# Kernel optimization log

Measured on AMD Instinct MI355X. Metric: run time of the kernel, lower is better.

## Reference

```python
import jax, jax.numpy as jnp
import numpy as np

EMB_DIM, TREE_DIM, OUT_DIM, VOCAB = 256, 256, 3, 10000
T, B, LEVELS = 255, 128, 8  # complete binary tree of depth 8, 128 trees per input


def _build_forest():
    # node j = T-1-heap(j): root (heap 0) is the LAST node so stack_last_h picks the root.
    heap = np.arange(T)
    depth = np.floor(np.log2(heap + 1)).astype(np.int64)  # 0..7
    node_order = np.empty(T, dtype=np.int64)
    node_order[T - 1 - heap] = (LEVELS - 1) - depth       # leaves=0, root=7
    internal = np.arange((T - 1) // 2)                     # heaps with two children
    parent = np.repeat(T - 1 - internal, 2)
    child = np.stack([T - 1 - (2 * internal + 1), T - 1 - (2 * internal + 2)], 1).reshape(-1)
    edges = np.stack([parent, child], axis=1)              # (254, 2)
    edge_order = node_order[parent]
    offs = (np.arange(B) * T)[:, None, None]
    adj = (edges[None] + offs).reshape(-1, 2)              # (B*254, 2)
    return np.tile(node_order, B), adj, np.tile(edge_order, B)


def setup_inputs() -> dict:
    key = jax.random.key(0)
    ks = jax.random.split(key, 16)
    no, adj, eo = _build_forest()
    D = TREE_DIM
    s_e = 1.0 / np.sqrt(EMB_DIM)
    s_t = 1.0 / np.sqrt(D)
    return {
        'feat_cube': jax.random.randint(ks[0], (B * T,), 0, VOCAB),
        'feat_a': jax.random.randint(ks[1], (B * T,), 0, VOCAB),
        'feat_b': jax.random.randint(ks[2], (B * T,), 0, VOCAB),
        'node_order': jnp.asarray(no),
        'adjacency_list': jnp.asarray(adj),
        'edge_order': jnp.asarray(eo),
        'num_levels': LEVELS,
        'num_trees': B,
        'emb': jax.random.normal(ks[3], (VOCAB, EMB_DIM), jnp.float32),
        'W_iou': jax.random.normal(ks[4], (3 * D, EMB_DIM), jnp.float32) * s_e,
        'b_iou': jnp.zeros((3 * D,), jnp.float32),
        'U_iou': jax.random.normal(ks[5], (3 * D, D), jnp.float32) * s_t,
        'W_f': jax.random.normal(ks[6], (D, EMB_DIM), jnp.float32) * s_e,
        'b_f': jnp.zeros((D,), jnp.float32),
        'U_f': jax.random.normal(ks[7], (D, D), jnp.float32) * s_t,
        'fc1_w': jax.random.normal(ks[8], (D // 2, D), jnp.float32) * s_t,
        'fc1_b': jnp.zeros((D // 2,), jnp.float32),
        'fc2_w': jax.random.normal(ks[9], (OUT_DIM, D // 2), jnp.float32) * (1.0 / np.sqrt(D // 2)),
        'fc2_b': jnp.zeros((OUT_DIM,), jnp.float32),
    }


def _tree_lstm(x, node_order, parents, children, edge_order, W_iou, b_iou, U_iou, W_f, b_f, U_f, num_levels):
    # Child-sum TreeLSTM, evaluated level by level (leaves first). Dense masked
    # formulation: per level we update only nodes with node_order==lvl; edge
    # contributions are masked before segment_sum (same math as the torch loop).
    N = x.shape[0]
    D = U_f.shape[0]
    x_iou = x @ W_iou.T + b_iou            # (N, 3D), precomputed once
    x_f = x @ W_f.T + b_f                  # (N, D)
    h = jnp.zeros((N, D), x.dtype)
    c = jnp.zeros((N, D), x.dtype)
    for lvl in range(num_levels):
        emask = (edge_order == lvl)[:, None].astype(x.dtype)
        ch = h[children]                   # (E, D) gather of child hidden
        cc = c[children]
        f = jax.nn.sigmoid(x_f[parents] + ch @ U_f.T)
        h_sum = jax.ops.segment_sum(ch * emask, parents, num_segments=N)
        c_sum = jax.ops.segment_sum(f * cc * emask, parents, num_segments=N)
        i, o, u = jnp.split(x_iou + h_sum @ U_iou.T, 3, axis=1)
        c_new = jax.nn.sigmoid(i) * jnp.tanh(u) + c_sum
        h_new = jax.nn.sigmoid(o) * jnp.tanh(c_new)
        nmask = (node_order == lvl)[:, None]
        h = jnp.where(nmask, h_new, h)
        c = jnp.where(nmask, c_new, c)
    return h, c


def reference(feat_cube, feat_a, feat_b, node_order, adjacency_list, edge_order,
              num_levels, num_trees, emb, W_iou, b_iou, U_iou, W_f, b_f, U_f,
              fc1_w, fc1_b, fc2_w, fc2_b):
    parents = adjacency_list[:, 0]
    children = adjacency_list[:, 1]

    def run_tree(feat):
        h, _ = _tree_lstm(emb[feat], node_order, parents, children, edge_order,
                          W_iou, b_iou, U_iou, W_f, b_f, U_f, num_levels)
        # stack_last_h: last node of each tree (= root with our labeling)
        return h.reshape(num_trees, -1, h.shape[-1])[:, -1, :]

    h_c = run_tree(feat_cube)
    h_a = run_tree(feat_a)
    h_b = run_tree(feat_b)
    # h_c (1,D) @ (h_a (D,1) @ h_b (1,D)) == (h_c . h_a) * h_b, fused einsum
    h = jnp.einsum('bi,bi,bj->bj', h_c, h_a, h_b)
    hid = jax.nn.relu(h @ fc1_w.T + fc1_b)
    logits = jax.nn.relu(hid @ fc2_w.T + fc2_b)
    return logits  # (num_trees, out_dim)
```

## Files before the change

### kernel.cpp

```cpp
#include <hip/hip_runtime.h>
#include <hip/hip_bf16.h>

typedef __hip_bfloat16 bf16;
typedef unsigned short u16;
typedef __attribute__((ext_vector_type(8))) short s8;
typedef __attribute__((ext_vector_type(4))) float f4;

#define NRUNS 3
#define NTREE 128
#define TT    255
#define DD    256
#define VPAD  10016
#define PAD   258

__device__ __forceinline__ float bits2f(u16 b){ union{unsigned u; float f;} x; x.u = ((unsigned)b)<<16; return x.f; }
__device__ __forceinline__ u16   f2bits(float f){ bf16 h = __float2bfloat16(f); return *(u16*)&h; }
__device__ __forceinline__ float sigm(float x){ return 1.f/(1.f+__expf(-x)); }
__device__ __forceinline__ float tanh_(float x){ return 1.f - 2.f/(__expf(2.f*x)+1.f); }

__global__ void k_detect(const u16* __restrict__ raw, int* __restrict__ flag){
    int t = threadIdx.x;
    int hit = 0;
    if (t < 128){
        u16 w = raw[2*t];
        int e = (w >> 7) & 0xFF;
        hit = (e >= 100 && e <= 141) ? 1 : 0;
    }
    __shared__ int cnt;
    if (t == 0) cnt = 0;
    __syncthreads();
    atomicAdd(&cnt, hit);
    __syncthreads();
    if (t == 0) flag[0] = (cnt >= 64) ? 1 : 0;
}

__device__ __forceinline__ u16 cvt1b(const void* p, int i, int isb){
    return isb ? ((const u16*)p)[i] : f2bits(((const float*)p)[i]);
}
__device__ __forceinline__ float cvt1f(const void* p, int i, int isb){
    return isb ? bits2f(((const u16*)p)[i]) : ((const float*)p)[i];
}

#define L_EMB  (10000*256)
#define L_EMBP (VPAD*256)
#define L_WIOU (768*256)
#define L_UIOU (768*256)
#define L_WF   (256*256)
#define L_UF   (256*256)
#define L_ALL  (L_EMBP + L_WIOU + L_UIOU + L_WF + L_UF)
#define S_BIOU 768
#define S_BF   256
#define S_F1W  (128*256)
#define S_F1B  128
#define S_F2W  (3*128)
#define S_F2B  3
#define S_ALL  (S_BIOU+S_BF+S_F1W+S_F1B+S_F2W+S_F2B)
__global__ void k_cvtall(const void* __restrict__ s0, const void* __restrict__ s1,
                         const void* __restrict__ s2, const void* __restrict__ s3,
                         const void* __restrict__ s4,
                         const void* __restrict__ t0, const void* __restrict__ t1,
                         const void* __restrict__ t2, const void* __restrict__ t3,
                         const void* __restrict__ t4, const void* __restrict__ t5,
                         u16* __restrict__ d0, u16* __restrict__ d1, u16* __restrict__ d2,
                         u16* __restrict__ d3, u16* __restrict__ d4,
                         float* __restrict__ e0, float* __restrict__ e1, float* __restrict__ e2,
                         float* __restrict__ e3, float* __restrict__ e4, float* __restrict__ e5,
                         const int* __restrict__ flag){
    int isb = flag[0];
    for (int i = blockIdx.x*blockDim.x + threadIdx.x; i < L_ALL + S_ALL; i += gridDim.x*blockDim.x){
        int j = i;
        if (j < L_EMBP){ d0[j] = (j < L_EMB) ? cvt1b(s0, j, isb) : (u16)0; continue; } j -= L_EMBP;
        if (j < L_WIOU){ d1[j] = cvt1b(s1, j, isb); continue; } j -= L_WIOU;
        if (j < L_UIOU){ d2[j] = cvt1b(s2, j, isb); continue; } j -= L_UIOU;
        if (j < L_WF){ d3[j] = cvt1b(s3, j, isb); continue; } j -= L_WF;
        if (j < L_UF){ d4[j] = cvt1b(s4, j, isb); continue; } j -= L_UF;
        if (j < S_BIOU){ e0[j] = cvt1f(t0, j, isb); continue; } j -= S_BIOU;
        if (j < S_BF){ e1[j] = cvt1f(t1, j, isb); continue; } j -= S_BF;
        if (j < S_F1W){ e2[j] = cvt1f(t2, j, isb); continue; } j -= S_F1W;
        if (j < S_F1B){ e3[j] = cvt1f(t3, j, isb); continue; } j -= S_F1B;
        if (j < S_F2W){ e4[j] = cvt1f(t4, j, isb); continue; } j -= S_F2W;
        e5[j] = cvt1f(t5, j, isb);
    }
}

__device__ __forceinline__ s8 ldB16(const u16* p){
    union { uint4 q; s8 v; } u;
    u.q = *(const uint4*)p;
    return u.v;
}
__device__ __forceinline__ s8 ldsA(const u16* p){
    union { unsigned w[4]; s8 v; } u;
    u.w[0] = *(const unsigned*)(p);
    u.w[1] = *(const unsigned*)(p+2);
    u.w[2] = *(const unsigned*)(p+4);
    u.w[3] = *(const unsigned*)(p+6);
    return u.v;
}
#define MFMA(acc,a,b) acc = __builtin_amdgcn_mfma_f32_16x16x32_bf16(a, b, acc, 0, 0, 0)

__global__ __launch_bounds__(512, 4)
void k_vocab2(const u16* __restrict__ embb,
              const u16* __restrict__ Wiou, const u16* __restrict__ Wfm,
              const u16* __restrict__ Ufm,  const float* __restrict__ biou_f,
              u16* __restrict__ E_iou, u16* __restrict__ E_f,
              u16* __restrict__ H0, u16* __restrict__ C0, u16* __restrict__ HU0)
{
    __shared__ u16 hs[32*PAD];
    const int t = threadIdx.x, w = t>>6, lane = t&63, ln = lane&15, q = lane>>4;
    const int r0 = blockIdx.x*32, d0 = w*32;

    const u16* Bp[8];
    #pragma unroll
    for (int g = 0; g < 4; g++)
      #pragma unroll
      for (int nc = 0; nc < 2; nc++){
        int nn = d0 + nc*16 + ln;
        Bp[g*2+nc] = (g < 3) ? (Wiou + (size_t)(g*256+nn)*DD) : (Wfm + (size_t)nn*DD);
      }
    const u16* a0p = embb + (size_t)(r0+ln)*DD;
    const u16* a1p = embb + (size_t)(r0+16+ln)*DD;
    f4 acc[8][2];
    #pragma unroll
    for (int nt = 0; nt < 8; nt++){ acc[nt][0] = (f4){0,0,0,0}; acc[nt][1] = (f4){0,0,0,0}; }
    #pragma unroll 2
    for (int ks = 0; ks < 8; ks++){
        int ko = ks*32 + q*8;
        s8 a0 = ldB16(a0p + ko);
        s8 a1 = ldB16(a1p + ko);
        #pragma unroll
        for (int nt = 0; nt < 8; nt++){
            s8 bb = ldB16(Bp[nt] + ko);
            MFMA(acc[nt][0], a0, bb);
            MFMA(acc[nt][1], a1, bb);
        }
    }
    #pragma unroll
    for (int nc = 0; nc < 2; nc++){
        int d = d0 + nc*16 + ln;
        float bi = biou_f[d], bo = biou_f[256+d], bu = biou_f[512+d];
        #pragma unroll
        for (int ms = 0; ms < 2; ms++)
          #pragma unroll
          for (int r = 0; r < 4; r++){
            int vrow = r0 + ms*16 + q*4 + r;
            float ei = acc[0*2+nc][ms][r];
            float eo = acc[1*2+nc][ms][r];
            float eu = acc[2*2+nc][ms][r];
            float ef = acc[3*2+nc][ms][r];
            size_t eb = (size_t)vrow*768 + d;
            E_iou[eb]       = f2bits(ei);
            E_iou[eb + 256] = f2bits(eo);
            E_iou[eb + 512] = f2bits(eu);
            E_f[(size_t)vrow*DD + d] = f2bits(ef);
            float cc = sigm(ei + bi)*tanh_(eu + bu);
            float hh = sigm(eo + bo)*tanh_(cc);
            C0[(size_t)vrow*DD + d] = f2bits(cc);
            H0[(size_t)vrow*DD + d] = f2bits(hh);
            hs[(ms*16 + q*4 + r)*PAD + d] = f2bits(hh);
        }
    }
    __syncthreads();

    f4 hacc[2][2];
    #pragma unroll
    for (int nt = 0; nt < 2; nt++){ hacc[nt][0] = (f4){0,0,0,0}; hacc[nt][1] = (f4){0,0,0,0}; }
    const u16* Bf0 = Ufm + (size_t)(d0 + ln)*DD;
    const u16* Bf1 = Ufm + (size_t)(d0 + 16 + ln)*DD;
    #pragma unroll 2
    for (int ks = 0; ks < 8; ks++){
        int ko = ks*32 + q*8;
        s8 a0 = ldsA(&hs[ln*PAD + ko]);
        s8 a1 = ldsA(&hs[(16+ln)*PAD + ko]);
        s8 b0 = ldB16(Bf0 + ko);
        s8 b1 = ldB16(Bf1 + ko);
        MFMA(hacc[0][0], a0, b0); MFMA(hacc[0][1], a1, b0);
        MFMA(hacc[1][0], a0, b1); MFMA(hacc[1][1], a1, b1);
    }
    #pragma unroll
    for (int nc = 0; nc < 2; nc++){
        int d = d0 + nc*16 + ln;
        #pragma unroll
        for (int ms = 0; ms < 2; ms++)
          #pragma unroll
          for (int r = 0; r < 4; r++){
            int vrow = r0 + ms*16 + q*4 + r;
            HU0[(size_t)vrow*DD + d] = f2bits(hacc[nc][ms][r]);
        }
    }
}

__global__ __launch_bounds__(512, 4)
void k_lvl1(const int* __restrict__ f0, const int* __restrict__ f1, const int* __restrict__ f2,
            const u16* __restrict__ E_iou, const u16* __restrict__ E_f,
            const u16* __restrict__ H0, const u16* __restrict__ C0, const u16* __restrict__ HU0,
            const u16* __restrict__ Uiou, const u16* __restrict__ Ufm,
            const float* __restrict__ biou_f, const float* __restrict__ bf_f,
            u16* __restrict__ hsum_out, u16* __restrict__ fcsum_out)
{
    __shared__ u16 hs[32*PAD];
    const int t = threadIdx.x, w = t>>6, lane = t&63, ln = lane&15, q = lane>>4;
    const int r0 = blockIdx.x*32, d0 = w*32;

    const u16 *pa1[2], *pa2[2];
    #pragma unroll
    for (int ms = 0; ms < 2; ms++){
        int row = r0 + ms*16 + ln;
        int run = row >> 13, rem = row & 8191;
        int b = rem >> 6, jj = rem & 63;
        const int* fp = (run==0) ? f0 : ((run==1) ? f1 : f2);
        pa1[ms] = H0 + (size_t)fp[b*TT + 2*jj]*DD;
        pa2[ms] = H0 + (size_t)fp[b*TT + 2*jj + 1]*DD;
    }
    int fo[2][4], v1e[2][4], v2e[2][4], featp[2][2];
    #pragma unroll
    for (int ms = 0; ms < 2; ms++)
      #pragma unroll
      for (int r = 0; r < 4; r++){
        int rho = r0 + ms*16 + q*4 + r;
        int run = rho >> 13, rem = rho & 8191;
        int b = rem >> 6, jj = rem & 63;
        const int* fp = (run==0) ? f0 : ((run==1) ? f1 : f2);
        fo[ms][r]  = fp[b*TT + 128 + jj];
        v1e[ms][r] = fp[b*TT + 2*jj];
        v2e[ms][r] = fp[b*TT + 2*jj + 1];
        if ((r&1)==0) featp[ms][r>>1] = fp[b*TT + 192 + (jj>>1)];
      }

    f4 acc[6][2];
    #pragma unroll
    for (int nt = 0; nt < 6; nt++){ acc[nt][0] = (f4){0,0,0,0}; acc[nt][1] = (f4){0,0,0,0}; }
    {
        const u16* Bp[6];
        #pragma unroll
        for (int nt = 0; nt < 6; nt++){
            int n = (nt>>1)*256 + d0 + (nt&1)*16 + ln;
            Bp[nt] = Uiou + (size_t)n*DD;
        }
        #pragma unroll 2
        for (int ks = 0; ks < 8; ks++){
            int ko = ks*32 + q*8;
            s8 a10 = ldB16(pa1[0] + ko);
            s8 a11 = ldB16(pa1[1] + ko);
            s8 a20 = ldB16(pa2[0] + ko);
            s8 a21 = ldB16(pa2[1] + ko);
            #pragma unroll
            for (int nt = 0; nt < 6; nt++){
                s8 bb = ldB16(Bp[nt] + ko);
                MFMA(acc[nt][0], a10, bb);
                MFMA(acc[nt][0], a20, bb);
                MFMA(acc[nt][1], a11, bb);
                MFMA(acc[nt][1], a21, bb);
            }
        }
    }

    float cv[2][2][4];
    #pragma unroll
    for (int nc = 0; nc < 2; nc++){
        int d = d0 + nc*16 + ln;
        float bi = biou_f[d], bo = biou_f[256+d], bu = biou_f[512+d];
        float bfv = bf_f[d];
        #pragma unroll
        for (int ms = 0; ms < 2; ms++){
            float hv[4];
            #pragma unroll
            for (int r = 0; r < 4; r++){
                size_t eb = (size_t)fo[ms][r]*768 + d;
                float iv = acc[0+nc][ms][r] + bits2f(E_iou[eb])       + bi;
                float ov = acc[2+nc][ms][r] + bits2f(E_iou[eb + 256]) + bo;
                float uv = acc[4+nc][ms][r] + bits2f(E_iou[eb + 512]) + bu;
                float e  = bits2f(E_f[(size_t)fo[ms][r]*DD + d]) + bfv;
                size_t b1 = (size_t)v1e[ms][r]*DD + d;
                size_t b2 = (size_t)v2e[ms][r]*DD + d;
                float fa = sigm(e + bits2f(HU0[b1]));
                float fb = sigm(e + bits2f(HU0[b2]));
                float cs = fa*bits2f(C0[b1]) + fb*bits2f(C0[b2]);
                float c = sigm(iv)*tanh_(uv) + cs;
                float h = sigm(ov)*tanh_(c);
                cv[nc][ms][r] = c;
                hv[r] = h;
                hs[(ms*16 + q*4 + r)*PAD + d] = f2bits(h);
            }
            int prow = (r0>>1) + ms*8 + q*2;
            hsum_out[(size_t)prow*DD + d]     = f2bits(hv[0] + hv[1]);
            hsum_out[(size_t)(prow+1)*DD + d] = f2bits(hv[2] + hv[3]);
        }
    }

    __syncthreads();
    f4 hacc[2][2];
    #pragma unroll
    for (int nt = 0; nt < 2; nt++){ hacc[nt][0] = (f4){0,0,0,0}; hacc[nt][1] = (f4){0,0,0,0}; }
    const u16* Bf0 = Ufm + (size_t)(d0 + ln)*DD;
    const u16* Bf1 = Ufm + (size_t)(d0 + 16 + ln)*DD;
    #pragma unroll 2
    for (int ks = 0; ks < 8; ks++){
        int ko = ks*32 + q*8;
        s8 a0 = ldsA(&hs[ln*PAD + ko]);
        s8 a1 = ldsA(&hs[(16+ln)*PAD + ko]);
        s8 b0 = ldB16(Bf0 + ko);
        s8 b1 = ldB16(Bf1 + ko);
        MFMA(hacc[0][0], a0, b0); MFMA(hacc[0][1], a1, b0);
        MFMA(hacc[1][0], a0, b1); MFMA(hacc[1][1], a1, b1);
    }
    #pragma unroll
    for (int nc = 0; nc < 2; nc++){
        int d = d0 + nc*16 + ln;
        float bfv = bf_f[d];
        #pragma unroll
        for (int ms = 0; ms < 2; ms++){
            float fs0, fs1;
            #pragma unroll
            for (int r = 0; r < 4; r++){
                float ef = bits2f(E_f[(size_t)featp[ms][r>>1]*DD + d]);
                float fc = sigm(ef + bfv + hacc[nc][ms][r]) * cv[nc][ms][r];
                if (r == 0) fs0 = fc;
                else if (r == 1) fs0 += fc;
                else if (r == 2) fs1 = fc;
                else fs1 += fc;
            }
            int prow = (r0>>1) + ms*8 + q*2;
            fcsum_out[(size_t)prow*DD + d]     = f2bits(fs0);
            fcsum_out[(size_t)(prow+1)*DD + d] = f2bits(fs1);
        }
    }
}

__global__ __launch_bounds__(512, 4)
void k_lvl(int lvl, int cLog,
           const int* __restrict__ f0, const int* __restrict__ f1, const int* __restrict__ f2,
           const u16* __restrict__ E_iou, const u16* __restrict__ E_f,
           const u16* __restrict__ Uiou, const u16* __restrict__ Ufm,
           const float* __restrict__ biou_f, const float* __restrict__ bf_f,
           const u16* __restrict__ hsum_in, const u16* __restrict__ fcsum_in,
           u16* __restrict__ hsum_out, u16* __restrict__ fcsum_out,
           u16* __restrict__ hroot)
{
    __shared__ u16 hs[32*PAD];
    const int t = threadIdx.x, w = t>>6, lane = t&63, ln = lane&15, q = lane>>4;
    const int cnt = 1 << cLog, S = 256 - 2*cnt;
    const int r0 = blockIdx.x*32, d0 = w*32;
    const bool haveP = (lvl < 7);

    int feat[2][4], featp[2][2];
    #pragma unroll
    for (int ms = 0; ms < 2; ms++)
      #pragma unroll
      for (int r = 0; r < 4; r++){
        int rho = r0 + ms*16 + q*4 + r;
        int run = rho >> (7+cLog);
        int rem = rho & ((1<<(7+cLog)) - 1);
        int b = rem >> cLog, jj = rem & (cnt-1);
        const int* fp = (run==0) ? f0 : ((run==1) ? f1 : f2);
        feat[ms][r] = fp[b*TT + S + jj];
        if (haveP && (r&1)==0)
            featp[ms][r>>1] = fp[b*TT + (256-cnt) + (jj>>1)];
      }

    f4 acc[6][2];
    #pragma unroll
    for (int nt = 0; nt < 6; nt++){ acc[nt][0] = (f4){0,0,0,0}; acc[nt][1] = (f4){0,0,0,0}; }
    {
        const u16* a0p = hsum_in + (size_t)(r0+ln)*DD;
        const u16* a1p = hsum_in + (size_t)(r0+16+ln)*DD;
        const u16* Bp[6];
        #pragma unroll
        for (int nt = 0; nt < 6; nt++){
            int n = (nt>>1)*256 + d0 + (nt&1)*16 + ln;
            Bp[nt] = Uiou + (size_t)n*DD;
        }
        #pragma unroll 2
        for (int ks = 0; ks < 8; ks++){
            int ko = ks*32 + q*8;
            s8 a0 = ldB16(a0p + ko);
            s8 a1 = ldB16(a1p + ko);
            #pragma unroll
            for (int nt = 0; nt < 6; nt++){
                s8 bb = ldB16(Bp[nt] + ko);
                MFMA(acc[nt][0], a0, bb);
                MFMA(acc[nt][1], a1, bb);
            }
        }
    }

    float cv[2][2][4];
    #pragma unroll
    for (int nc = 0; nc < 2; nc++){
        int d = d0 + nc*16 + ln;
        float bi = biou_f[d], bo = biou_f[256+d], bu = biou_f[512+d];
        #pragma unroll
        for (int ms = 0; ms < 2; ms++){
            float hv[4];
            #pragma unroll
            for (int r = 0; r < 4; r++){
                int rho = r0 + ms*16 + q*4 + r;
                size_t eb = (size_t)feat[ms][r]*768 + d;
                float iv = acc[0+nc][ms][r] + bits2f(E_iou[eb])       + bi;
                float ov = acc[2+nc][ms][r] + bits2f(E_iou[eb + 256]) + bo;
                float uv = acc[4+nc][ms][r] + bits2f(E_iou[eb + 512]) + bu;
                float cs = bits2f(fcsum_in[(size_t)rho*DD + d]);
                float c = sigm(iv)*tanh_(uv) + cs;
                float h = sigm(ov)*tanh_(c);
                cv[nc][ms][r] = c;
                hv[r] = h;
                if (haveP) hs[(ms*16 + q*4 + r)*PAD + d] = f2bits(h);
                else       hroot[(size_t)rho*DD + d] = f2bits(h);
            }
            if (haveP){
                int prow = (r0>>1) + ms*8 + q*2;
                hsum_out[(size_t)prow*DD + d]     = f2bits(hv[0] + hv[1]);
                hsum_out[(size_t)(prow+1)*DD + d] = f2bits(hv[2] + hv[3]);
            }
        }
    }

    if (haveP){
        __syncthreads();
        f4 hacc[2][2];
        #pragma unroll
        for (int nt = 0; nt < 2; nt++){ hacc[nt][0] = (f4){0,0,0,0}; hacc[nt][1] = (f4){0,0,0,0}; }
        const u16* Bf0 = Ufm + (size_t)(d0 + ln)*DD;
        const u16* Bf1 = Ufm + (size_t)(d0 + 16 + ln)*DD;
        #pragma unroll 2
        for (int ks = 0; ks < 8; ks++){
            int ko = ks*32 + q*8;
            s8 a0 = ldsA(&hs[ln*PAD + ko]);
            s8 a1 = ldsA(&hs[(16+ln)*PAD + ko]);
            s8 b0 = ldB16(Bf0 + ko);
            s8 b1 = ldB16(Bf1 + ko);
            MFMA(hacc[0][0], a0, b0); MFMA(hacc[0][1], a1, b0);
            MFMA(hacc[1][0], a0, b1); MFMA(hacc[1][1], a1, b1);
        }
        #pragma unroll
        for (int nc = 0; nc < 2; nc++){
            int d = d0 + nc*16 + ln;
            float bfv = bf_f[d];
            #pragma unroll
            for (int ms = 0; ms < 2; ms++){
                float fs0, fs1;
                #pragma unroll
                for (int r = 0; r < 4; r++){
                    float ef = bits2f(E_f[(size_t)featp[ms][r>>1]*DD + d]);
                    float fc = sigm(ef + bfv + hacc[nc][ms][r]) * cv[nc][ms][r];
                    if (r == 0) fs0 = fc;
                    else if (r == 1) fs0 += fc;
                    else if (r == 2) fs1 = fc;
                    else fs1 += fc;
                }
                int prow = (r0>>1) + ms*8 + q*2;
                fcsum_out[(size_t)prow*DD + d]     = f2bits(fs0);
                fcsum_out[(size_t)(prow+1)*DD + d] = f2bits(fs1);
            }
        }
    }
}

__global__ __launch_bounds__(256)
void k_final(const u16* __restrict__ hroot,
             const float* __restrict__ fc1w, const float* __restrict__ fc1b,
             const float* __restrict__ fc2w, const float* __restrict__ fc2b,
             void* __restrict__ out, const int* __restrict__ flag)
{
    int b = blockIdx.x, t = threadIdx.x;
    __shared__ float sprod[DD];
    __shared__ float shb[DD];
    __shared__ float shid[128];
    float hc  = bits2f(hroot[(0*NTREE + b)*DD + t]);
    float ha  = bits2f(hroot[(1*NTREE + b)*DD + t]);
    float hbv = bits2f(hroot[(2*NTREE + b)*DD + t]);
    sprod[t] = hc * ha;
    shb[t]   = hbv;
    __syncthreads();
    for (int s = 128; s > 0; s >>= 1){
        if (t < s) sprod[t] += sprod[t + s];
        __syncthreads();
    }
    float dot = sprod[0];
    if (t < 128){
        float acc = fc1b[t];
        for (int k = 0; k < DD; k++)
            acc = fmaf(dot * shb[k], fc1w[t*DD + k], acc);
        shid[t] = fmaxf(acc, 0.f);
    }
    __syncthreads();
    if (t < 3){
        float acc = fc2b[t];
        for (int j = 0; j < 128; j++)
            acc = fmaf(fc2w[t*128 + j], shid[j], acc);
        float v = fmaxf(acc, 0.f);
        if (flag[0]) ((bf16*)out)[b*3 + t] = __float2bfloat16(v);
        else         ((float*)out)[b*3 + t] = v;
    }
}

extern "C" void kernel_launch(void* const* d_in, const int* in_sizes, int n_in,
                              void* d_out, int out_size, void* d_ws, size_t ws_size,
                              hipStream_t stream)
{
    const int* f0 = (const int*)d_in[0];
    const int* f1 = (const int*)d_in[1];
    const int* f2 = (const int*)d_in[2];
    const void* emb  = d_in[8];
    const void* Wiou = d_in[9];
    const void* biou = d_in[10];
    const void* Uiou = d_in[11];
    const void* Wf   = d_in[12];
    const void* bfv  = d_in[13];
    const void* Uf   = d_in[14];
    const void* fc1w = d_in[15];
    const void* fc1b = d_in[16];
    const void* fc2w = d_in[17];
    const void* fc2b = d_in[18];

    char* base = (char*)d_ws;
    size_t off = 0;
    auto take = [&](size_t bytes) -> char* {
        char* p = base + off;
        off = (off + bytes + 255) & ~(size_t)255;
        return p;
    };
    int*   flag   = (int*)  take(256);
    u16*   embb   = (u16*)  take((size_t)L_EMBP*2);
    u16*   wioub  = (u16*)  take((size_t)L_WIOU*2);
    u16*   uioub  = (u16*)  take((size_t)L_UIOU*2);
    u16*   wfb    = (u16*)  take((size_t)L_WF*2);
    u16*   ufb    = (u16*)  take((size_t)L_UF*2);
    float* biou_f = (float*)take(S_BIOU*4);
    float* bf_f   = (float*)take(S_BF*4);
    float* fc1w_f = (float*)take(S_F1W*4);
    float* fc1b_f = (float*)take(S_F1B*4);
    float* fc2w_f = (float*)take(S_F2W*4);
    float* fc2b_f = (float*)take(S_F2B*4);
    u16*   E_iou  = (u16*)  take((size_t)VPAD*768*2);
    u16*   E_f    = (u16*)  take((size_t)VPAD*DD*2);
    u16*   H0     = (u16*)  take((size_t)VPAD*DD*2);
    u16*   C0     = (u16*)  take((size_t)VPAD*DD*2);
    u16*   HU0    = (u16*)  take((size_t)VPAD*DD*2);
    u16*   HB     = (u16*)  take((size_t)12288*DD*2);
    u16*   FB     = (u16*)  take((size_t)12288*DD*2);
    u16*   HA     = (u16*)  take((size_t)6144*DD*2);
    u16*   FA     = (u16*)  take((size_t)6144*DD*2);
    u16*   hroot  = (u16*)  take((size_t)NRUNS*NTREE*DD*2);

    k_detect<<<1, 256, 0, stream>>>((const u16*)emb, flag);
    k_cvtall<<<2048, 256, 0, stream>>>(emb, Wiou, Uiou, Wf, Uf,
                                       biou, bfv, fc1w, fc1b, fc2w, fc2b,
                                       embb, wioub, uioub, wfb, ufb,
                                       biou_f, bf_f, fc1w_f, fc1b_f, fc2w_f, fc2b_f, flag);
    k_vocab2<<<VPAD/32, 512, 0, stream>>>(embb, wioub, wfb, ufb, biou_f,
                                          E_iou, E_f, H0, C0, HU0);
    k_lvl1<<<768, 512, 0, stream>>>(f0, f1, f2, E_iou, E_f, H0, C0, HU0,
                                    uioub, ufb, biou_f, bf_f, HB, FB);

    for (int lvl = 2; lvl <= 7; lvl++){
        int cLog = 7 - lvl;
        int rows = NRUNS*NTREE*(128 >> lvl);
        int blocks = rows / 32;
        int pe = lvl & 1;
        u16* hs_o = pe ? HB : HA;
        u16* fc_o = pe ? FB : FA;
        const u16* hs_i = pe ? HA : HB;
        const u16* fc_i = pe ? FA : FB;
        k_lvl<<<blocks, 512, 0, stream>>>(lvl, cLog, f0, f1, f2,
                                          E_iou, E_f, uioub, ufb,
                                          biou_f, bf_f,
                                          hs_i, fc_i, hs_o, fc_o, hroot);
    }
    k_final<<<NTREE, 256, 0, stream>>>(hroot, fc1w_f, fc1b_f, fc2w_f, fc2b_f, d_out, flag);
}
```

Before: 472.1 us.

## Fuse all tree levels into one persistent per-tree kernel using LDS ping-pong

Replaces the level-1 kernel and six per-level launches with a single kernel where each block processes one whole tree across all levels. Intermediate child-sum h and forget-gated c sums stay in shared-memory ping-pong buffers instead of round-tripping through global memory. Level 1 is restructured to precompute the child sums first and run one MFMA pass instead of two. The cost is only 384 blocks with large LDS use, which lowers parallelism. Upper levels still compute full 32-row tiles even when only a few nodes are valid.

```diff
diff --git a/kernel.cpp b/kernel.cpp
--- a/kernel.cpp
+++ b/kernel.cpp
@@ -190,190 +190,76 @@
 }
 
 __global__ __launch_bounds__(512, 4)
-void k_lvl1(const int* __restrict__ f0, const int* __restrict__ f1, const int* __restrict__ f2,
+void k_tree(const int* __restrict__ f0, const int* __restrict__ f1, const int* __restrict__ f2,
             const u16* __restrict__ E_iou, const u16* __restrict__ E_f,
             const u16* __restrict__ H0, const u16* __restrict__ C0, const u16* __restrict__ HU0,
             const u16* __restrict__ Uiou, const u16* __restrict__ Ufm,
             const float* __restrict__ biou_f, const float* __restrict__ bf_f,
-            u16* __restrict__ hsum_out, u16* __restrict__ fcsum_out)
+            u16* __restrict__ hroot)
 {
-    __shared__ u16 hs[32*PAD];
+    __shared__ u16 bufH[2][32*PAD];
+    __shared__ u16 bufF[2][32*PAD];
     const int t = threadIdx.x, w = t>>6, lane = t&63, ln = lane&15, q = lane>>4;
-    const int r0 = blockIdx.x*32, d0 = w*32;
-
-    const u16 *pa1[2], *pa2[2];
+    const int d0 = w*32;
+    const int tb = blockIdx.x;
+    const int run = tb >> 7, b = tb & 127;
+    const int* fp = (run==0) ? f0 : ((run==1) ? f1 : f2);
+    const int base = b*TT;
+
+    const u16* Bp[6];
     #pragma unroll
-    for (int ms = 0; ms < 2; ms++){
-        int row = r0 + ms*16 + ln;
-        int run = row >> 13, rem = row & 8191;
-        int b = rem >> 6, jj = rem & 63;
-        const int* fp = (run==0) ? f0 : ((run==1) ? f1 : f2);
-        pa1[ms] = H0 + (size_t)fp[b*TT + 2*jj]*DD;
-        pa2[ms] = H0 + (size_t)fp[b*TT + 2*jj + 1]*DD;
-    }
-    int fo[2][4], v1e[2][4], v2e[2][4], featp[2][2];
-    #pragma unroll
-    for (int ms = 0; ms < 2; ms++)
-      #pragma unroll
-      for (int r = 0; r < 4; r++){
-        int rho = r0 + ms*16 + q*4 + r;
-        int run = rho >> 13, rem = rho & 8191;
-        int b = rem >> 6, jj = rem & 63;
-        const int* fp = (run==0) ? f0 : ((run==1) ? f1 : f2);
-        fo[ms][r]  = fp[b*TT + 128 + jj];
-        v1e[ms][r] = fp[b*TT + 2*jj];
-        v2e[ms][r] = fp[b*TT + 2*jj + 1];
-        if ((r&1)==0) featp[ms][r>>1] = fp[b*TT + 192 + (jj>>1)];
-      }
-
-    f4 acc[6][2];
-    #pragma unroll
-    for (int nt = 0; nt < 6; nt++){ acc[nt][0] = (f4){0,0,0,0}; acc[nt][1] = (f4){0,0,0,0}; }
-    {
-        const u16* Bp[6];
-        #pragma unroll
-        for (int nt = 0; nt < 6; nt++){
-            int n = (nt>>1)*256 + d0 + (nt&1)*16 + ln;
-            Bp[nt] = Uiou + (size_t)n*DD;
-        }
+    for (int nt = 0; nt < 6; nt++){
+        int n = (nt>>1)*256 + d0 + (nt&1)*16 + ln;
+        Bp[nt] = Uiou + (size_t)n*DD;
+    }
+    const u16* Bf0 = Ufm + (size_t)(d0 + ln)*DD;
+    const u16* Bf1 = Ufm + (size_t)(d0 + 16 + ln)*DD;
+
+    for (int half = 0; half < 2; half++){
+        {
+            int row = t >> 4, c = t & 15;
+            int jj = half*32 + row;
+            int fo_ = fp[base + 128 + jj];
+            int v1  = fp[base + 2*jj];
+            int v2  = fp[base + 2*jj + 1];
+            int dd  = c*16;
+            const u16* pe  = E_f + (size_t)fo_*DD + dd;
+            const u16* ph1 = H0  + (size_t)v1*DD + dd;
+            const u16* ph2 = H0  + (size_t)v2*DD + dd;
+            const u16* pc1 = C0  + (size_t)v1*DD + dd;
+            const u16* pc2 = C0  + (size_t)v2*DD + dd;
+            const u16* pu1 = HU0 + (size_t)v1*DD + dd;
+            const u16* pu2 = HU0 + (size_t)v2*DD + dd;
+            #pragma unroll
+            for (int g = 0; g < 2; g++){
+                int o = g*8;
+                s8 ef  = ldB16(pe + o);
+                s8 h1  = ldB16(ph1 + o), h2 = ldB16(ph2 + o);
+                s8 c1  = ldB16(pc1 + o), c2 = ldB16(pc2 + o);
+                s8 hu1 = ldB16(pu1 + o), hu2 = ldB16(pu2 + o);
+                union { u16 a[8]; uint4 q4; } uh, uf;
+                #pragma unroll
+                for (int j = 0; j < 8; j++){
+                    float e  = bits2f((u16)ef[j]) + bf_f[dd + o + j];
+                    float fa = sigm(e + bits2f((u16)hu1[j]));
+                    float fb = sigm(e + bits2f((u16)hu2[j]));
+                    uf.a[j] = f2bits(fa*bits2f((u16)c1[j]) + fb*bits2f((u16)c2[j]));
+                    uh.a[j] = f2bits(bits2f((u16)h1[j]) + bits2f((u16)h2[j]));
+                }
+                *(uint4*)&bufH[0][row*PAD + dd + o] = uh.q4;
+                *(uint4*)&bufF[0][row*PAD + dd + o] = uf.q4;
+            }
+        }
+        __syncthreads();
+
+        f4 acc[6][2];
+        #pragma unroll
+        for (int nt = 0; nt < 6; nt++){ acc[nt][0] = (f4){0,0,0,0}; acc[nt][1] = (f4){0,0,0,0}; }
         #pragma unroll 2
         for (int ks = 0; ks < 8; ks++){
             int ko = ks*32 + q*8;
-            s8 a10 = ldB16(pa1[0] + ko);
-            s8 a11 = ldB16(pa1[1] + ko);
-            s8 a20 = ldB16(pa2[0] + ko);
-            s8 a21 = ldB16(pa2[1] + ko);
-            #pragma unroll
-            for (int nt = 0; nt < 6; nt++){
-                s8 bb = ldB16(Bp[nt] + ko);
-                MFMA(acc[nt][0], a10, bb);
-                MFMA(acc[nt][0], a20, bb);
-                MFMA(acc[nt][1], a11, bb);
-                MFMA(acc[nt][1], a21, bb);
-            }
-        }
-    }
-
-    float cv[2][2][4];
-    #pragma unroll
-    for (int nc = 0; nc < 2; nc++){
-        int d = d0 + nc*16 + ln;
-        float bi = biou_f[d], bo = biou_f[256+d], bu = biou_f[512+d];
-        float bfv = bf_f[d];
-        #pragma unroll
-        for (int ms = 0; ms < 2; ms++){
-            float hv[4];
-            #pragma unroll
-            for (int r = 0; r < 4; r++){
-                size_t eb = (size_t)fo[ms][r]*768 + d;
-                float iv = acc[0+nc][ms][r] + bits2f(E_iou[eb])       + bi;
-                float ov = acc[2+nc][ms][r] + bits2f(E_iou[eb + 256]) + bo;
-                float uv = acc[4+nc][ms][r] + bits2f(E_iou[eb + 512]) + bu;
-                float e  = bits2f(E_f[(size_t)fo[ms][r]*DD + d]) + bfv;
-                size_t b1 = (size_t)v1e[ms][r]*DD + d;
-                size_t b2 = (size_t)v2e[ms][r]*DD + d;
-                float fa = sigm(e + bits2f(HU0[b1]));
-                float fb = sigm(e + bits2f(HU0[b2]));
-                float cs = fa*bits2f(C0[b1]) + fb*bits2f(C0[b2]);
-                float c = sigm(iv)*tanh_(uv) + cs;
-                float h = sigm(ov)*tanh_(c);
-                cv[nc][ms][r] = c;
-                hv[r] = h;
-                hs[(ms*16 + q*4 + r)*PAD + d] = f2bits(h);
-            }
-            int prow = (r0>>1) + ms*8 + q*2;
-            hsum_out[(size_t)prow*DD + d]     = f2bits(hv[0] + hv[1]);
-            hsum_out[(size_t)(prow+1)*DD + d] = f2bits(hv[2] + hv[3]);
-        }
-    }
-
-    __syncthreads();
-    f4 hacc[2][2];
-    #pragma unroll
-    for (int nt = 0; nt < 2; nt++){ hacc[nt][0] = (f4){0,0,0,0}; hacc[nt][1] = (f4){0,0,0,0}; }
-    const u16* Bf0 = Ufm + (size_t)(d0 + ln)*DD;
-    const u16* Bf1 = Ufm + (size_t)(d0 + 16 + ln)*DD;
-    #pragma unroll 2
-    for (int ks = 0; ks < 8; ks++){
-        int ko = ks*32 + q*8;
-        s8 a0 = ldsA(&hs[ln*PAD + ko]);
-        s8 a1 = ldsA(&hs[(16+ln)*PAD + ko]);
-        s8 b0 = ldB16(Bf0 + ko);
-        s8 b1 = ldB16(Bf1 + ko);
-        MFMA(hacc[0][0], a0, b0); MFMA(hacc[0][1], a1, b0);
-        MFMA(hacc[1][0], a0, b1); MFMA(hacc[1][1], a1, b1);
-    }
-    #pragma unroll
-    for (int nc = 0; nc < 2; nc++){
-        int d = d0 + nc*16 + ln;
-        float bfv = bf_f[d];
-        #pragma unroll
-        for (int ms = 0; ms < 2; ms++){
-            float fs0, fs1;
-            #pragma unroll
-            for (int r = 0; r < 4; r++){
-                float ef = bits2f(E_f[(size_t)featp[ms][r>>1]*DD + d]);
-                float fc = sigm(ef + bfv + hacc[nc][ms][r]) * cv[nc][ms][r];
-                if (r == 0) fs0 = fc;
-                else if (r == 1) fs0 += fc;
-                else if (r == 2) fs1 = fc;
-                else fs1 += fc;
-            }
-            int prow = (r0>>1) + ms*8 + q*2;
-            fcsum_out[(size_t)prow*DD + d]     = f2bits(fs0);
-            fcsum_out[(size_t)(prow+1)*DD + d] = f2bits(fs1);
-        }
-    }
-}
-
-__global__ __launch_bounds__(512, 4)
-void k_lvl(int lvl, int cLog,
-           const int* __restrict__ f0, const int* __restrict__ f1, const int* __restrict__ f2,
-           const u16* __restrict__ E_iou, const u16* __restrict__ E_f,
-           const u16* __restrict__ Uiou, const u16* __restrict__ Ufm,
-           const float* __restrict__ biou_f, const float* __restrict__ bf_f,
-           const u16* __restrict__ hsum_in, const u16* __restrict__ fcsum_in,
-           u16* __restrict__ hsum_out, u16* __restrict__ fcsum_out,
-           u16* __restrict__ hroot)
-{
-    __shared__ u16 hs[32*PAD];
-    const int t = threadIdx.x, w = t>>6, lane = t&63, ln = lane&15, q = lane>>4;
-    const int cnt = 1 << cLog, S = 256 - 2*cnt;
-    const int r0 = blockIdx.x*32, d0 = w*32;
-    const bool haveP = (lvl < 7);
-
-    int feat[2][4], featp[2][2];
-    #pragma unroll
-    for (int ms = 0; ms < 2; ms++)
-      #pragma unroll
-      for (int r = 0; r < 4; r++){
-        int rho = r0 + ms*16 + q*4 + r;
-        int run = rho >> (7+cLog);
-        int rem = rho & ((1<<(7+cLog)) - 1);
-        int b = rem >> cLog, jj = rem & (cnt-1);
-        const int* fp = (run==0) ? f0 : ((run==1) ? f1 : f2);
-        feat[ms][r] = fp[b*TT + S + jj];
-        if (haveP && (r&1)==0)
-            featp[ms][r>>1] = fp[b*TT + (256-cnt) + (jj>>1)];
-      }
-
-    f4 acc[6][2];
-    #pragma unroll
-    for (int nt = 0; nt < 6; nt++){ acc[nt][0] = (f4){0,0,0,0}; acc[nt][1] = (f4){0,0,0,0}; }
-    {
-        const u16* a0p = hsum_in + (size_t)(r0+ln)*DD;
-        const u16* a1p = hsum_in + (size_t)(r0+16+ln)*DD;
-        const u16* Bp[6];
-        #pragma unroll
-        for (int nt = 0; nt < 6; nt++){
-            int n = (nt>>1)*256 + d0 + (nt&1)*16 + ln;
-            Bp[nt] = Uiou + (size_t)n*DD;
-        }
-        #pragma unroll 2
-        for (int ks = 0; ks < 8; ks++){
-            int ko = ks*32 + q*8;
-            s8 a0 = ldB16(a0p + ko);
-            s8 a1 = ldB16(a1p + ko);
+            s8 a0 = ldsA(&bufH[0][ln*PAD + ko]);
+            s8 a1 = ldsA(&bufH[0][(16+ln)*PAD + ko]);
             #pragma unroll
             for (int nt = 0; nt < 6; nt++){
                 s8 bb = ldB16(Bp[nt] + ko);
@@ -381,51 +267,46 @@
                 MFMA(acc[nt][1], a1, bb);
             }
         }
-    }
-
-    float cv[2][2][4];
-    #pragma unroll
-    for (int nc = 0; nc < 2; nc++){
-        int d = d0 + nc*16 + ln;
-        float bi = biou_f[d], bo = biou_f[256+d], bu = biou_f[512+d];
-        #pragma unroll
-        for (int ms = 0; ms < 2; ms++){
-            float hv[4];
-            #pragma unroll
-            for (int r = 0; r < 4; r++){
-                int rho = r0 + ms*16 + q*4 + r;
-                size_t eb = (size_t)feat[ms][r]*768 + d;
-                float iv = acc[0+nc][ms][r] + bits2f(E_iou[eb])       + bi;
-                float ov = acc[2+nc][ms][r] + bits2f(E_iou[eb + 256]) + bo;
-                float uv = acc[4+nc][ms][r] + bits2f(E_iou[eb + 512]) + bu;
-                float cs = bits2f(fcsum_in[(size_t)rho*DD + d]);
-                float c = sigm(iv)*tanh_(uv) + cs;
-                float h = sigm(ov)*tanh_(c);
-                cv[nc][ms][r] = c;
-                hv[r] = h;
-                if (haveP) hs[(ms*16 + q*4 + r)*PAD + d] = f2bits(h);
-                else       hroot[(size_t)rho*DD + d] = f2bits(h);
-            }
-            if (haveP){
-                int prow = (r0>>1) + ms*8 + q*2;
-                hsum_out[(size_t)prow*DD + d]     = f2bits(hv[0] + hv[1]);
-                hsum_out[(size_t)(prow+1)*DD + d] = f2bits(hv[2] + hv[3]);
-            }
-        }
-    }
-
-    if (haveP){
-        __syncthreads();
+        __syncthreads();
+
+        float cv[2][2][4];
+        #pragma unroll
+        for (int nc = 0; nc < 2; nc++){
+            int d = d0 + nc*16 + ln;
+            float bi = biou_f[d], bo = biou_f[256+d], bu = biou_f[512+d];
+            #pragma unroll
+            for (int ms = 0; ms < 2; ms++){
+                float hv[4];
+                #pragma unroll
+                for (int r = 0; r < 4; r++){
+                    int m  = ms*16 + q*4 + r;
+                    int jj = half*32 + m;
+                    size_t eb = (size_t)fp[base + 128 + jj]*768 + d;
+                    float iv = acc[0+nc][ms][r] + bits2f(E_iou[eb])       + bi;
+                    float ov = acc[2+nc][ms][r] + bits2f(E_iou[eb + 256]) + bo;
+                    float uv = acc[4+nc][ms][r] + bits2f(E_iou[eb + 512]) + bu;
+                    float cs = bits2f(bufF[0][m*PAD + d]);
+                    float c = sigm(iv)*tanh_(uv) + cs;
+                    float h = sigm(ov)*tanh_(c);
+                    cv[nc][ms][r] = c;
+                    hv[r] = h;
+                    bufH[0][m*PAD + d] = f2bits(h);
+                }
+                int prow = half*16 + ms*8 + q*2;
+                bufH[1][prow*PAD + d]     = f2bits(hv[0] + hv[1]);
+                bufH[1][(prow+1)*PAD + d] = f2bits(hv[2] + hv[3]);
+            }
+        }
+        __syncthreads();
+
         f4 hacc[2][2];
         #pragma unroll
         for (int nt = 0; nt < 2; nt++){ hacc[nt][0] = (f4){0,0,0,0}; hacc[nt][1] = (f4){0,0,0,0}; }
-        const u16* Bf0 = Ufm + (size_t)(d0 + ln)*DD;
-        const u16* Bf1 = Ufm + (size_t)(d0 + 16 + ln)*DD;
         #pragma unroll 2
         for (int ks = 0; ks < 8; ks++){
             int ko = ks*32 + q*8;
-            s8 a0 = ldsA(&hs[ln*PAD + ko]);
-            s8 a1 = ldsA(&hs[(16+ln)*PAD + ko]);
+            s8 a0 = ldsA(&bufH[0][ln*PAD + ko]);
+            s8 a1 = ldsA(&bufH[0][(16+ln)*PAD + ko]);
             s8 b0 = ldB16(Bf0 + ko);
             s8 b1 = ldB16(Bf1 + ko);
             MFMA(hacc[0][0], a0, b0); MFMA(hacc[0][1], a1, b0);
@@ -440,18 +321,122 @@
                 float fs0, fs1;
                 #pragma unroll
                 for (int r = 0; r < 4; r++){
-                    float ef = bits2f(E_f[(size_t)featp[ms][r>>1]*DD + d]);
+                    int jj = half*32 + ms*16 + q*4 + r;
+                    float ef = bits2f(E_f[(size_t)fp[base + 192 + (jj>>1)]*DD + d]);
                     float fc = sigm(ef + bfv + hacc[nc][ms][r]) * cv[nc][ms][r];
                     if (r == 0) fs0 = fc;
                     else if (r == 1) fs0 += fc;
                     else if (r == 2) fs1 = fc;
                     else fs1 += fc;
                 }
-                int prow = (r0>>1) + ms*8 + q*2;
-                fcsum_out[(size_t)prow*DD + d]     = f2bits(fs0);
-                fcsum_out[(size_t)(prow+1)*DD + d] = f2bits(fs1);
-            }
-        }
+                int prow = half*16 + ms*8 + q*2;
+                bufF[1][prow*PAD + d]     = f2bits(fs0);
+                bufF[1][(prow+1)*PAD + d] = f2bits(fs1);
+            }
+        }
+        __syncthreads();
+    }
+
+    int inI = 1;
+    for (int lvl = 2; lvl <= 7; lvl++){
+        const int cnt = 128 >> lvl;
+        const int S   = 256 - 2*cnt;
+        const int outI = inI ^ 1;
+        u16* hsIn  = bufH[inI];
+        u16* fcIn  = bufF[inI];
+        u16* hsOut = bufH[outI];
+        u16* fcOut = bufF[outI];
+        const int half_out = cnt >> 1;
+
+        f4 acc[6][2];
+        #pragma unroll
+        for (int nt = 0; nt < 6; nt++){ acc[nt][0] = (f4){0,0,0,0}; acc[nt][1] = (f4){0,0,0,0}; }
+        #pragma unroll 2
+        for (int ks = 0; ks < 8; ks++){
+            int ko = ks*32 + q*8;
+            s8 a0 = ldsA(&hsIn[ln*PAD + ko]);
+            s8 a1 = ldsA(&hsIn[(16+ln)*PAD + ko]);
+            #pragma unroll
+            for (int nt = 0; nt < 6; nt++){
+                s8 bb = ldB16(Bp[nt] + ko);
+                MFMA(acc[nt][0], a0, bb);
+                MFMA(acc[nt][1], a1, bb);
+            }
+        }
+        __syncthreads();
+
+        float cv[2][2][4];
+        #pragma unroll
+        for (int nc = 0; nc < 2; nc++){
+            int d = d0 + nc*16 + ln;
+            float bi = biou_f[d], bo = biou_f[256+d], bu = biou_f[512+d];
+            #pragma unroll
+            for (int ms = 0; ms < 2; ms++){
+                float hv[4];
+                #pragma unroll
+                for (int r = 0; r < 4; r++){
+                    int m   = ms*16 + q*4 + r;
+                    int jjc = (m < cnt) ? m : (cnt - 1);
+                    size_t eb = (size_t)fp[base + S + jjc]*768 + d;
+                    float iv = acc[0+nc][ms][r] + bits2f(E_iou[eb])       + bi;
+                    float ov = acc[2+nc][ms][r] + bits2f(E_iou[eb + 256]) + bo;
+                    float uv = acc[4+nc][ms][r] + bits2f(E_iou[eb + 512]) + bu;
+                    float cs = bits2f(fcIn[m*PAD + d]);
+                    float c = sigm(iv)*tanh_(uv) + cs;
+                    float h = sigm(ov)*tanh_(c);
+                    cv[nc][ms][r] = c;
+                    hv[r] = h;
+                    hsIn[m*PAD + d] = f2bits(h);
+                    if (lvl == 7 && m == 0)
+                        hroot[(size_t)tb*DD + d] = f2bits(h);
+                }
+                int prow = ms*8 + q*2;
+                if (prow < half_out)     hsOut[prow*PAD + d]     = f2bits(hv[0] + hv[1]);
+                if (prow+1 < half_out)   hsOut[(prow+1)*PAD + d] = f2bits(hv[2] + hv[3]);
+            }
+        }
+        __syncthreads();
+
+        if (lvl < 7){
+            f4 hacc[2][2];
+            #pragma unroll
+            for (int nt = 0; nt < 2; nt++){ hacc[nt][0] = (f4){0,0,0,0}; hacc[nt][1] = (f4){0,0,0,0}; }
+            #pragma unroll 2
+            for (int ks = 0; ks < 8; ks++){
+                int ko = ks*32 + q*8;
+                s8 a0 = ldsA(&hsIn[ln*PAD + ko]);
+                s8 a1 = ldsA(&hsIn[(16+ln)*PAD + ko]);
+                s8 b0 = ldB16(Bf0 + ko);
+                s8 b1 = ldB16(Bf1 + ko);
+                MFMA(hacc[0][0], a0, b0); MFMA(hacc[0][1], a1, b0);
+                MFMA(hacc[1][0], a0, b1); MFMA(hacc[1][1], a1, b1);
+            }
+            #pragma unroll
+            for (int nc = 0; nc < 2; nc++){
+                int d = d0 + nc*16 + ln;
+                float bfv = bf_f[d];
+                #pragma unroll
+                for (int ms = 0; ms < 2; ms++){
+                    float fs0, fs1;
+                    #pragma unroll
+                    for (int r = 0; r < 4; r++){
+                        int m   = ms*16 + q*4 + r;
+                        int jjc = (m < cnt) ? m : (cnt - 1);
+                        float ef = bits2f(E_f[(size_t)fp[base + (256-cnt) + (jjc>>1)]*DD + d]);
+                        float fc = sigm(ef + bfv + hacc[nc][ms][r]) * cv[nc][ms][r];
+                        if (r == 0) fs0 = fc;
+                        else if (r == 1) fs0 += fc;
+                        else if (r == 2) fs1 = fc;
+                        else fs1 += fc;
+                    }
+                    int prow = ms*8 + q*2;
+                    if (prow < half_out)   fcOut[prow*PAD + d]     = f2bits(fs0);
+                    if (prow+1 < half_out) fcOut[(prow+1)*PAD + d] = f2bits(fs1);
+                }
+            }
+            __syncthreads();
+        }
+        inI = outI;
     }
 }
 
@@ -536,10 +521,6 @@
     u16*   H0     = (u16*)  take((size_t)VPAD*DD*2);
     u16*   C0     = (u16*)  take((size_t)VPAD*DD*2);
     u16*   HU0    = (u16*)  take((size_t)VPAD*DD*2);
-    u16*   HB     = (u16*)  take((size_t)12288*DD*2);
-    u16*   FB     = (u16*)  take((size_t)12288*DD*2);
-    u16*   HA     = (u16*)  take((size_t)6144*DD*2);
-    u16*   FA     = (u16*)  take((size_t)6144*DD*2);
     u16*   hroot  = (u16*)  take((size_t)NRUNS*NTREE*DD*2);
 
     k_detect<<<1, 256, 0, stream>>>((const u16*)emb, flag);
@@ -549,22 +530,7 @@
                                        biou_f, bf_f, fc1w_f, fc1b_f, fc2w_f, fc2b_f, flag);
     k_vocab2<<<VPAD/32, 512, 0, stream>>>(embb, wioub, wfb, ufb, biou_f,
                                           E_iou, E_f, H0, C0, HU0);
-    k_lvl1<<<768, 512, 0, stream>>>(f0, f1, f2, E_iou, E_f, H0, C0, HU0,
-                                    uioub, ufb, biou_f, bf_f, HB, FB);
-
-    for (int lvl = 2; lvl <= 7; lvl++){
-        int cLog = 7 - lvl;
-        int rows = NRUNS*NTREE*(128 >> lvl);
-        int blocks = rows / 32;
-        int pe = lvl & 1;
-        u16* hs_o = pe ? HB : HA;
-        u16* fc_o = pe ? FB : FA;
-        const u16* hs_i = pe ? HA : HB;
-        const u16* fc_i = pe ? FA : FB;
-        k_lvl<<<blocks, 512, 0, stream>>>(lvl, cLog, f0, f1, f2,
-                                          E_iou, E_f, uioub, ufb,
-                                          biou_f, bf_f,
-                                          hs_i, fc_i, hs_o, fc_o, hroot);
-    }
+    k_tree<<<NRUNS*NTREE, 512, 0, stream>>>(f0, f1, f2, E_iou, E_f, H0, C0, HU0,
+                                            uioub, ufb, biou_f, bf_f, hroot);
     k_final<<<NTREE, 256, 0, stream>>>(hroot, fc1w_f, fc1b_f, fc2w_f, fc2b_f, d_out, flag);
 }
```

Result: slower. 488.5 us (+3.5%).
